# Kernel optimization log

Hardware: AMD Instinct MI355X
Metric: run time of the kernel (lower is better)

The kernel has to match this reference:

```python
import jax, jax.numpy as jnp
import numpy as np

GN_EPS = 1e-5
GN_GROUPS = 8
KNN_EPS = 1e-8


def group_norm(x, w, b):
    # x: [B, C, N]
    B, C, N = x.shape
    xg = x.reshape(B, GN_GROUPS, C // GN_GROUPS, N)
    mu = jnp.mean(xg, axis=(2, 3), keepdims=True)
    var = jnp.var(xg, axis=(2, 3), keepdims=True)
    xg = (xg - mu) * jax.lax.rsqrt(var + GN_EPS)
    return xg.reshape(B, C, N) * w[None, :, None] + b[None, :, None]


def swish(x):
    return x * jax.nn.sigmoid(x)


def three_interpolate(points_coords, centers_coords, centers_features):
    # points_coords [B,3,N], centers_coords [B,3,M], centers_features [B,C,M]
    B, _, N = points_coords.shape
    C = centers_features.shape[1]
    p2 = jnp.sum(points_coords ** 2, axis=1)            # [B,N]
    c2 = jnp.sum(centers_coords ** 2, axis=1)           # [B,M]
    cross = jnp.einsum('bdn,bdm->bnm', points_coords, centers_coords)
    dist2 = p2[:, :, None] + c2[:, None, :] - 2.0 * cross  # [B,N,M] squared dists
    neg_d, idx = jax.lax.top_k(-dist2, 3)               # 3 smallest -> [B,N,3]
    d = -neg_d
    w = 1.0 / (d + KNN_EPS)
    w = w / jnp.sum(w, axis=-1, keepdims=True)          # [B,N,3]
    featsT = jnp.swapaxes(centers_features, 1, 2)       # [B,M,C]
    gathered = jnp.take_along_axis(featsT, idx.reshape(B, N * 3, 1), axis=1)
    gathered = gathered.reshape(B, N, 3, C)
    out = jnp.einsum('bnk,bnkc->bcn', w, gathered)      # [B,C,N]
    return out


def setup_inputs() -> dict:
    key = jax.random.key(0)
    ks = jax.random.split(key, 8)
    B, N, M = 8, 8192, 2048
    C_ctr, C_pts, D = 256, 128, 64
    Cin, C1, C2 = C_ctr + C_pts, 256, 256
    return {
        'points_coords': jax.random.normal(ks[0], (B, 3, N), jnp.float32),
        'centers_coords': jax.random.normal(ks[1], (B, 3, M), jnp.float32),
        'centers_features': jax.random.normal(ks[2], (B, C_ctr, M), jnp.float32),
        'points_features': jax.random.normal(ks[3], (B, C_pts, N), jnp.float32),
        'time_emb': jax.random.normal(ks[4], (B, D, 1), jnp.float32),
        'W1': jax.random.normal(ks[5], (C1, Cin), jnp.float32) * (1.0 / np.sqrt(Cin)),
        'b1': jnp.zeros((C1,), jnp.float32),
        'gn1_w': jnp.ones((C1,), jnp.float32),
        'gn1_b': jnp.zeros((C1,), jnp.float32),
        'W2': jax.random.normal(ks[6], (C2, C1), jnp.float32) * (1.0 / np.sqrt(C1)),
        'b2': jnp.zeros((C2,), jnp.float32),
        'gn2_w': jnp.ones((C2,), jnp.float32),
        'gn2_b': jnp.zeros((C2,), jnp.float32),
    }


def reference(points_coords, centers_coords, centers_features, points_features,
              time_emb, W1, b1, gn1_w, gn1_b, W2, b2, gn2_w, gn2_b):
    interp = three_interpolate(points_coords, centers_coords, centers_features)
    x = jnp.concatenate([interp, points_features], axis=1)  # [B, Cin, N]
    # SharedMLP layer 1: Conv1d(k=1) + GroupNorm(8) + Swish
    x = jnp.einsum('oc,bcn->bon', W1, x) + b1[None, :, None]
    x = swish(group_norm(x, gn1_w, gn1_b))
    # layer 2
    x = jnp.einsum('oc,bcn->bon', W2, x) + b2[None, :, None]
    x = swish(group_norm(x, gn2_w, gn2_b))
    N = points_coords.shape[-1]
    time_emb_exp = jnp.broadcast_to(time_emb[:, :, 0:1], time_emb.shape[:2] + (N,))
    return (x, points_coords, time_emb_exp)
```

## Files before the change

kernel.cpp:

```cpp
#include <hip/hip_runtime.h>
#include <hip/hip_bf16.h>
#include <float.h>

#define B_ 8
#define N_ 8192
#define M_ 2048
#define CC_ 256
#define CP_ 128
#define CIN_ 384
#define GRP_ 8

typedef __attribute__((ext_vector_type(8))) short short8;
typedef __attribute__((ext_vector_type(4))) short short4v;
typedef __attribute__((ext_vector_type(4))) float f32x4;

static __device__ __forceinline__ float bf2f(unsigned short u) {
  union { unsigned int i; float f; } v; v.i = ((unsigned int)u) << 16; return v.f;
}
static __device__ __forceinline__ unsigned short f2bf(float f) {
  union { float f; unsigned int i; } v; v.f = f;
  unsigned int u = v.i;
  unsigned int r = (u + 0x7FFFu + ((u >> 16) & 1u)) >> 16;
  return (unsigned short)r;
}
static __device__ __forceinline__ void gload16(const void* g, void* l) {
  __builtin_amdgcn_global_load_lds(
      (const __attribute__((address_space(1))) void*)g,
      (__attribute__((address_space(3))) void*)l, 16, 0, 0);
}

__global__ __launch_bounds__(256) void k_prep(
    const float* __restrict__ W1, const float* __restrict__ W2,
    short* __restrict__ W1b, short* __restrict__ W2b,
    const float* __restrict__ cf, short* __restrict__ FT,
    const float* __restrict__ pf, short* __restrict__ x0T) {
  __shared__ float tile[32][33];
  int bid = blockIdx.x;
  int t = threadIdx.x;
  if (bid < 384) {
    int i = bid * 256 + t;
    if (i < 256 * CIN_) W1b[i] = (short)f2bf(W1[i]);
    if (i < 256 * 256)  W2b[i] = (short)f2bf(W2[i]);
    return;
  }
  const float* in; short* out;
  int C, Nn, RS, coff, n0, c0, b;
  if (bid < 4480) {
    int q = bid - 384;
    in = cf; out = FT; C = CC_; Nn = M_; RS = CC_; coff = 0;
    n0 = (q & 63) * 32; c0 = ((q >> 6) & 7) * 32; b = q >> 9;
  } else {
    int q = bid - 4480;
    in = pf; out = x0T; C = CP_; Nn = N_; RS = CIN_; coff = 256;
    n0 = (q & 255) * 32; c0 = ((q >> 8) & 3) * 32; b = q >> 10;
  }
  const float* inb = in + (size_t)b * C * Nn;
  short* outb = out + (size_t)b * Nn * RS;
  int tx = t & 31, ty = t >> 5;
#pragma unroll
  for (int i = 0; i < 32; i += 8)
    tile[ty + i][tx] = inb[(size_t)(c0 + ty + i) * Nn + n0 + tx];
  __syncthreads();
#pragma unroll
  for (int i = 0; i < 32; i += 8)
    outb[(size_t)(n0 + ty + i) * RS + coff + c0 + tx] = (short)f2bf(tile[tx][ty + i]);
}

__global__ __launch_bounds__(512) void k_knn(
    const float* __restrict__ pc, const float* __restrict__ cc,
    int* __restrict__ idx, float* __restrict__ wts) {
  __shared__ __align__(16) float4 ctr[M_];
  __shared__ double mk[8][3][128];
  int b = blockIdx.y;
  int t = threadIdx.x;
  const float* ccb = cc + (size_t)b * 3 * M_;
  for (int i = t; i < M_; i += 512) {
    float x = ccb[i], y = ccb[M_ + i], z = ccb[2 * M_ + i];
    ctr[i] = make_float4(x, y, z, x * x + y * y + z * z);
  }
  __syncthreads();
  int wv = t >> 6, lane = t & 63;
  int base = blockIdx.x * 128;
  const float* pcb = pc + (size_t)b * 3 * N_;
  int na = base + lane, nb = base + 64 + lane;
  float pxa = pcb[na], pya = pcb[N_ + na], pza = pcb[2 * N_ + na];
  float pxb = pcb[nb], pyb = pcb[N_ + nb], pzb = pcb[2 * N_ + nb];
  float p2a = pxa * pxa + pya * pya + pza * pza;
  float p2b = pxb * pxb + pyb * pyb + pzb * pzb;
  const double kinit = __hiloint2double(0x7F7FFFFF, 0);
  double a0 = kinit, a1 = kinit, a2 = kinit;
  double e0 = kinit, e1 = kinit, e2 = kinit;
  const float4* C = ctr + wv * 256;
  int mbase = wv * 256;
#pragma unroll 8
  for (int m = 0; m < 256; ++m) {
    float4 c = C[m];
    float dota = pxa * c.x;
    dota = __builtin_fmaf(pya, c.y, dota);
    dota = __builtin_fmaf(pza, c.z, dota);
    float da = __builtin_fmaf(-2.f, dota, c.w) + p2a;
    float dotb = pxb * c.x;
    dotb = __builtin_fmaf(pyb, c.y, dotb);
    dotb = __builtin_fmaf(pzb, c.z, dotb);
    float db = __builtin_fmaf(-2.f, dotb, c.w) + p2b;
    double ka = __hiloint2double(__float_as_int(da), mbase + m);
    double kb = __hiloint2double(__float_as_int(db), mbase + m);
    double t0 = fmin(ka, a0);
    double t1 = fmin(fmax(ka, a0), a1);
    double t2 = fmin(fmax(ka, a1), a2);
    a0 = t0; a1 = t1; a2 = t2;
    double u0 = fmin(kb, e0);
    double u1 = fmin(fmax(kb, e0), e1);
    double u2 = fmin(fmax(kb, e1), e2);
    e0 = u0; e1 = u1; e2 = u2;
  }
  mk[wv][0][lane] = a0; mk[wv][1][lane] = a1; mk[wv][2][lane] = a2;
  mk[wv][0][64 + lane] = e0; mk[wv][1][64 + lane] = e1; mk[wv][2][64 + lane] = e2;
  __syncthreads();
  if (t < 128) {
    double k0 = kinit, k1 = kinit, k2 = kinit;
#pragma unroll
    for (int w = 0; w < 8; ++w) {
#pragma unroll
      for (int j = 0; j < 3; ++j) {
        double key = mk[w][j][t];
        double n0 = fmin(key, k0);
        double n1 = fmin(fmax(key, k0), k1);
        double n2 = fmin(fmax(key, k1), k2);
        k0 = n0; k1 = n1; k2 = n2;
      }
    }
    float d0 = __int_as_float(__double2hiint(k0));
    float d1 = __int_as_float(__double2hiint(k1));
    float d2 = __int_as_float(__double2hiint(k2));
    float w0 = 1.f / (d0 + 1e-8f), w1 = 1.f / (d1 + 1e-8f), w2 = 1.f / (d2 + 1e-8f);
    float inv = 1.f / (w0 + w1 + w2);
    int bn = b * N_ + base + t;
    wts[bn] = w0 * inv; wts[B_ * N_ + bn] = w1 * inv; wts[2 * B_ * N_ + bn] = w2 * inv;
    idx[bn] = __double2loint(k0);
    idx[B_ * N_ + bn] = __double2loint(k1);
    idx[2 * B_ * N_ + bn] = __double2loint(k2);
  }
}

__global__ __launch_bounds__(256) void k_interp(
    const short* __restrict__ FT, const int* __restrict__ idx,
    const float* __restrict__ wts, short* __restrict__ x0T) {
  int b = blockIdx.y;
  int t = threadIdx.x;
  int nl = t >> 5, cch = (t & 31) * 8;
  int n = blockIdx.x * 8 + nl;
  int bn = b * N_ + n;
  int i0 = idx[bn], i1 = idx[B_ * N_ + bn], i2 = idx[2 * B_ * N_ + bn];
  float w0 = wts[bn], w1 = wts[B_ * N_ + bn], w2 = wts[2 * B_ * N_ + bn];
  const short* Fb = FT + (size_t)b * M_ * CC_;
  short8 f0 = *(const short8*)(Fb + (size_t)i0 * CC_ + cch);
  short8 f1 = *(const short8*)(Fb + (size_t)i1 * CC_ + cch);
  short8 f2 = *(const short8*)(Fb + (size_t)i2 * CC_ + cch);
  short8 r;
#pragma unroll
  for (int e = 0; e < 8; ++e) {
    float v = w0 * bf2f((unsigned short)f0[e]) + w1 * bf2f((unsigned short)f1[e]) +
              w2 * bf2f((unsigned short)f2[e]);
    r[e] = (short)f2bf(v);
  }
  *(short8*)(x0T + (size_t)bn * CIN_ + cch) = r;
}

__global__ __launch_bounds__(256) void k_gemm(
    const short* __restrict__ Wb, const short* __restrict__ Xb,
    const float* __restrict__ bias, short* __restrict__ Yb,
    float* __restrict__ part, int K) {
  __shared__ __align__(16) short sW[128 * 64];
  __shared__ __align__(16) short sX[128 * 64];
  int b = blockIdx.z;
  int otile = blockIdx.x * 128;
  int ntile = blockIdx.y * 128;
  int t = threadIdx.x;
  int wv = t >> 6, lane = t & 63;
  int wr = wv >> 1, wc = wv & 1;
  int fr = lane & 15;
  int g = lane >> 4;
  f32x4 acc[4][4] = {};
  const short* Wp = Wb + (size_t)otile * K;
  const short* Xp = Xb + ((size_t)b * N_ + ntile) * K;
  for (int k0 = 0; k0 < K; k0 += 64) {
#pragma unroll
    for (int j = 0; j < 4; ++j) {
      int s = j * 256 + t;
      int row = s >> 3;
      int kc = (s & 7) ^ (row & 7);
      gload16(Wp + (size_t)row * K + k0 + kc * 8, sW + j * 2048 + wv * 512);
      gload16(Xp + (size_t)row * K + k0 + kc * 8, sX + j * 2048 + wv * 512);
    }
    __syncthreads();
#pragma unroll
    for (int h = 0; h < 2; ++h) {
      short8 af[4], bfr[4];
#pragma unroll
      for (int m = 0; m < 4; ++m) {
        int ra = wr * 64 + m * 16 + fr;
        af[m] = *(const short8*)(sW + ra * 64 + (((h * 4 + g) ^ (ra & 7)) << 3));
        int rb = wc * 64 + m * 16 + fr;
        bfr[m] = *(const short8*)(sX + rb * 64 + (((h * 4 + g) ^ (rb & 7)) << 3));
      }
#pragma unroll
      for (int m = 0; m < 4; ++m)
#pragma unroll
        for (int nn = 0; nn < 4; ++nn)
          acc[m][nn] = __builtin_amdgcn_mfma_f32_16x16x32_bf16(af[m], bfr[nn], acc[m][nn], 0, 0, 0);
    }
    __syncthreads();
  }
  float s01 = 0.f, ss01 = 0.f, s23 = 0.f, ss23 = 0.f;
#pragma unroll
  for (int m = 0; m < 4; ++m) {
    int o = otile + wr * 64 + m * 16 + g * 4;
    float4 bi = *(const float4*)(bias + o);
#pragma unroll
    for (int nn = 0; nn < 4; ++nn) {
      int n = ntile + wc * 64 + nn * 16 + fr;
      float v0 = acc[m][nn][0] + bi.x;
      float v1 = acc[m][nn][1] + bi.y;
      float v2 = acc[m][nn][2] + bi.z;
      float v3 = acc[m][nn][3] + bi.w;
      if (m < 2) { s01 += v0 + v1 + v2 + v3; ss01 += v0*v0 + v1*v1 + v2*v2 + v3*v3; }
      else       { s23 += v0 + v1 + v2 + v3; ss23 += v0*v0 + v1*v1 + v2*v2 + v3*v3; }
      short4v sv;
      sv[0] = (short)f2bf(v0);
      sv[1] = (short)f2bf(v1);
      sv[2] = (short)f2bf(v2);
      sv[3] = (short)f2bf(v3);
      *(short4v*)(Yb + ((size_t)b * N_ + n) * 256 + o) = sv;
    }
  }
#pragma unroll
  for (int off = 32; off > 0; off >>= 1) {
    s01 += __shfl_down(s01, off);
    ss01 += __shfl_down(ss01, off);
    s23 += __shfl_down(s23, off);
    ss23 += __shfl_down(ss23, off);
  }
  float* wred = (float*)sW;
  if (lane == 0) {
    wred[wv * 4 + 0] = s01; wred[wv * 4 + 1] = ss01;
    wred[wv * 4 + 2] = s23; wred[wv * 4 + 3] = ss23;
  }
  __syncthreads();
  if (t < 8) {
    int gl = t >> 1, sel = t & 1;
    int wrn = gl >> 1;
    int id = (gl & 1) * 2 + sel;
    float v = wred[(wrn * 2 + 0) * 4 + id] + wred[(wrn * 2 + 1) * 4 + id];
    part[(((size_t)b * 8 + blockIdx.x * 4 + gl) * 64 + blockIdx.y) * 2 + sel] = v;
  }
}

__global__ __launch_bounds__(256) void k_gnapply(short* __restrict__ Y,
                                                 const float* __restrict__ part,
                                                 const float* __restrict__ gw,
                                                 const float* __restrict__ gb) {
  __shared__ float fs[128];
  int t = threadIdx.x;
  if (t < 64) {
    float s = 0.f, ss = 0.f;
    for (int j = 0; j < 64; ++j) {
      s += part[((size_t)t * 64 + j) * 2];
      ss += part[((size_t)t * 64 + j) * 2 + 1];
    }
    const float cnt = 32.f * 8192.f;
    float mean = s / cnt;
    float var = ss / cnt - mean * mean;
    fs[t * 2] = mean;
    fs[t * 2 + 1] = rsqrtf(var + 1e-5f);
  }
  __syncthreads();
  unsigned int* Yd = (unsigned int*)Y;
  int total = B_ * N_ * 128;
  for (int i = blockIdx.x * blockDim.x + t; i < total;
       i += gridDim.x * blockDim.x) {
    int o2 = i & 127;
    int b = i >> 20;
    int g = o2 >> 4;
    float mean = fs[(b * 8 + g) * 2], rstd = fs[(b * 8 + g) * 2 + 1];
    unsigned int v = Yd[i];
    int o = o2 * 2;
    float a = bf2f((unsigned short)(v & 0xFFFF));
    float c = bf2f((unsigned short)(v >> 16));
    a = (a - mean) * rstd * gw[o] + gb[o];
    c = (c - mean) * rstd * gw[o + 1] + gb[o + 1];
    a = a / (1.f + __expf(-a));
    c = c / (1.f + __expf(-c));
    Yd[i] = (unsigned int)f2bf(a) | ((unsigned int)f2bf(c) << 16);
  }
}

__global__ __launch_bounds__(256) void k_gnapply_out(
    const short* __restrict__ Y, const float* __restrict__ part,
    const float* __restrict__ gw, const float* __restrict__ gb,
    float* __restrict__ out) {
  __shared__ float tile[64][65];
  __shared__ float fs[16];
  int b = blockIdx.z;
  int t = threadIdx.x;
  if (t < 8) {
    float s = 0.f, ss = 0.f;
    for (int j = 0; j < 64; ++j) {
      s += part[(((size_t)b * 8 + t) * 64 + j) * 2];
      ss += part[(((size_t)b * 8 + t) * 64 + j) * 2 + 1];
    }
    const float cnt = 32.f * 8192.f;
    float mean = s / cnt;
    float var = ss / cnt - mean * mean;
    fs[t * 2] = mean;
    fs[t * 2 + 1] = rsqrtf(var + 1e-5f);
  }
  __syncthreads();
  int n0 = blockIdx.x * 64, o0 = blockIdx.y * 64;
  int row = t >> 5, dcol = t & 31;
  const unsigned int* Yd = (const unsigned int*)(Y + (size_t)b * N_ * 256);
  int o = o0 + dcol * 2;
  int g = o >> 5;
  float mean = fs[g * 2], rstd = fs[g * 2 + 1];
  float w0 = gw[o], w1 = gw[o + 1], bb0 = gb[o], bb1 = gb[o + 1];
#pragma unroll
  for (int p = 0; p < 8; ++p) {
    int n = n0 + p * 8 + row;
    unsigned int v = Yd[(size_t)n * 128 + (o0 >> 1) + dcol];
    float a = bf2f((unsigned short)(v & 0xFFFF));
    float c = bf2f((unsigned short)(v >> 16));
    a = (a - mean) * rstd * w0 + bb0; a = a / (1.f + __expf(-a));
    c = (c - mean) * rstd * w1 + bb1; c = c / (1.f + __expf(-c));
    tile[p * 8 + row][dcol * 2] = a;
    tile[p * 8 + row][dcol * 2 + 1] = c;
  }
  __syncthreads();
  int ol = t >> 2, nch = (t & 3) * 16;
  float* ob = out + ((size_t)(b * 256 + o0 + ol)) * N_ + n0 + nch;
#pragma unroll
  for (int c4 = 0; c4 < 16; c4 += 4) {
    float4 v4;
    v4.x = tile[nch + c4 + 0][ol];
    v4.y = tile[nch + c4 + 1][ol];
    v4.z = tile[nch + c4 + 2][ol];
    v4.w = tile[nch + c4 + 3][ol];
    *(float4*)(ob + c4) = v4;
  }
}

__global__ void k_tail(const float* __restrict__ pc, const float* __restrict__ te,
                       float* __restrict__ out) {
  int total = 196608 + B_ * 64 * N_;
  for (int i = blockIdx.x * blockDim.x + threadIdx.x; i < total;
       i += gridDim.x * blockDim.x) {
    if (i < 196608) {
      out[16777216 + i] = pc[i];
    } else {
      int j = i - 196608;
      int bd = j >> 13;
      out[16973824 + j] = te[bd];
    }
  }
}

extern "C" void kernel_launch(void* const* d_in, const int* in_sizes, int n_in,
                              void* d_out, int out_size, void* d_ws, size_t ws_size,
                              hipStream_t stream) {
  const float* pc  = (const float*)d_in[0];
  const float* cc  = (const float*)d_in[1];
  const float* cf  = (const float*)d_in[2];
  const float* pf  = (const float*)d_in[3];
  const float* te  = (const float*)d_in[4];
  const float* W1  = (const float*)d_in[5];
  const float* b1  = (const float*)d_in[6];
  const float* g1w = (const float*)d_in[7];
  const float* g1b = (const float*)d_in[8];
  const float* W2  = (const float*)d_in[9];
  const float* b2  = (const float*)d_in[10];
  const float* g2w = (const float*)d_in[11];
  const float* g2b = (const float*)d_in[12];
  float* out = (float*)d_out;

  char* ws = (char*)d_ws;
  size_t off = 0;
  auto alloc = [&](size_t bytes) {
    char* p = ws + off;
    off += (bytes + 255) & ~(size_t)255;
    return p;
  };
  short* FT   = (short*)alloc((size_t)B_ * M_ * CC_ * 2);
  short* x0T  = (short*)alloc((size_t)B_ * N_ * CIN_ * 2);
  short* y1   = (short*)alloc((size_t)B_ * N_ * 256 * 2);
  short* W1b  = (short*)alloc(256 * 384 * 2);
  short* W2b  = (short*)alloc(256 * 256 * 2);
  int*   idx  = (int*)alloc((size_t)3 * B_ * N_ * 4);
  float* wts  = (float*)alloc((size_t)3 * B_ * N_ * 4);
  float* part1 = (float*)alloc(8 * 8 * 64 * 2 * 4);
  float* part2 = (float*)alloc(8 * 8 * 64 * 2 * 4);
  short* y2 = (short*)x0T;

  k_prep<<<12672, 256, 0, stream>>>(W1, W2, W1b, W2b, cf, FT, pf, x0T);
  k_knn<<<dim3(N_ / 128, B_), 512, 0, stream>>>(pc, cc, idx, wts);
  k_interp<<<dim3(N_ / 8, B_), 256, 0, stream>>>(FT, idx, wts, x0T);
  k_gemm<<<dim3(2, N_ / 128, B_), 256, 0, stream>>>(W1b, x0T, b1, y1, part1, CIN_);
  k_gnapply<<<2048, 256, 0, stream>>>(y1, part1, g1w, g1b);
  k_gemm<<<dim3(2, N_ / 128, B_), 256, 0, stream>>>(W2b, y1, b2, y2, part2, 256);
  k_gnapply_out<<<dim3(N_ / 64, 4, B_), 256, 0, stream>>>(y2, part2, g2w, g2b, out);
  k_tail<<<2048, 256, 0, stream>>>(pc, te, out);
}
```

Measured before the change: 194.8 us.

## Merge prep, kNN and tail copy into one heterogeneous front kernel

Combines the weight/feature conversion, the kNN search and the passthrough output copy into a single launch, with the work type chosen by block index. Independent work can then share the GPU at once, which removes two launch gaps and lets the memory-bound transposes run beside the compute-bound kNN. In exchange every block reserves the union shared-memory footprint (56KB) and uses 512 threads, which can lower occupancy for the transpose blocks. The transpose now packs two 32x32 tiles per block.

```diff
diff --git a/kernel.cpp b/kernel.cpp
--- a/kernel.cpp
+++ b/kernel.cpp
@@ -29,117 +29,128 @@
       (__attribute__((address_space(3))) void*)l, 16, 0, 0);
 }
 
-__global__ __launch_bounds__(256) void k_prep(
+__global__ __launch_bounds__(512) void k_front(
+    const float* __restrict__ pc, const float* __restrict__ cc,
+    int* __restrict__ idx, float* __restrict__ wts,
     const float* __restrict__ W1, const float* __restrict__ W2,
     short* __restrict__ W1b, short* __restrict__ W2b,
     const float* __restrict__ cf, short* __restrict__ FT,
-    const float* __restrict__ pf, short* __restrict__ x0T) {
-  __shared__ float tile[32][33];
+    const float* __restrict__ pf, short* __restrict__ x0T,
+    const float* __restrict__ te, float* __restrict__ out) {
+  __shared__ __align__(16) char smem[57344];
   int bid = blockIdx.x;
   int t = threadIdx.x;
-  if (bid < 384) {
-    int i = bid * 256 + t;
+  if (bid < 512) {
+    float4* ctr = (float4*)smem;
+    double (*mk)[3][128] = (double(*)[3][128])(smem + 32768);
+    int b = bid >> 6;
+    int base = (bid & 63) * 128;
+    const float* ccb = cc + (size_t)b * 3 * M_;
+    for (int i = t; i < M_; i += 512) {
+      float x = ccb[i], y = ccb[M_ + i], z = ccb[2 * M_ + i];
+      ctr[i] = make_float4(x, y, z, x * x + y * y + z * z);
+    }
+    __syncthreads();
+    int wv = t >> 6, lane = t & 63;
+    const float* pcb = pc + (size_t)b * 3 * N_;
+    int na = base + lane, nb = base + 64 + lane;
+    float pxa = pcb[na], pya = pcb[N_ + na], pza = pcb[2 * N_ + na];
+    float pxb = pcb[nb], pyb = pcb[N_ + nb], pzb = pcb[2 * N_ + nb];
+    float p2a = pxa * pxa + pya * pya + pza * pza;
+    float p2b = pxb * pxb + pyb * pyb + pzb * pzb;
+    const double kinit = __hiloint2double(0x7F7FFFFF, 0);
+    double a0 = kinit, a1 = kinit, a2 = kinit;
+    double e0 = kinit, e1 = kinit, e2 = kinit;
+    const float4* C = ctr + wv * 256;
+    int mbase = wv * 256;
+#pragma unroll 8
+    for (int m = 0; m < 256; ++m) {
+      float4 c = C[m];
+      float dota = pxa * c.x;
+      dota = __builtin_fmaf(pya, c.y, dota);
+      dota = __builtin_fmaf(pza, c.z, dota);
+      float da = __builtin_fmaf(-2.f, dota, c.w) + p2a;
+      float dotb = pxb * c.x;
+      dotb = __builtin_fmaf(pyb, c.y, dotb);
+      dotb = __builtin_fmaf(pzb, c.z, dotb);
+      float db = __builtin_fmaf(-2.f, dotb, c.w) + p2b;
+      double ka = __hiloint2double(__float_as_int(da), mbase + m);
+      double kb = __hiloint2double(__float_as_int(db), mbase + m);
+      double t0 = fmin(ka, a0);
+      double t1 = fmin(fmax(ka, a0), a1);
+      double t2 = fmin(fmax(ka, a1), a2);
+      a0 = t0; a1 = t1; a2 = t2;
+      double u0 = fmin(kb, e0);
+      double u1 = fmin(fmax(kb, e0), e1);
+      double u2 = fmin(fmax(kb, e1), e2);
+      e0 = u0; e1 = u1; e2 = u2;
+    }
+    mk[wv][0][lane] = a0; mk[wv][1][lane] = a1; mk[wv][2][lane] = a2;
+    mk[wv][0][64 + lane] = e0; mk[wv][1][64 + lane] = e1; mk[wv][2][64 + lane] = e2;
+    __syncthreads();
+    if (t < 128) {
+      double k0 = kinit, k1 = kinit, k2 = kinit;
+#pragma unroll
+      for (int w = 0; w < 8; ++w) {
+#pragma unroll
+        for (int j = 0; j < 3; ++j) {
+          double key = mk[w][j][t];
+          double n0 = fmin(key, k0);
+          double n1 = fmin(fmax(key, k0), k1);
+          double n2 = fmin(fmax(key, k1), k2);
+          k0 = n0; k1 = n1; k2 = n2;
+        }
+      }
+      float d0 = __int_as_float(__double2hiint(k0));
+      float d1 = __int_as_float(__double2hiint(k1));
+      float d2 = __int_as_float(__double2hiint(k2));
+      float w0 = 1.f / (d0 + 1e-8f), w1 = 1.f / (d1 + 1e-8f), w2 = 1.f / (d2 + 1e-8f);
+      float inv = 1.f / (w0 + w1 + w2);
+      int bn = b * N_ + base + t;
+      wts[bn] = w0 * inv; wts[B_ * N_ + bn] = w1 * inv; wts[2 * B_ * N_ + bn] = w2 * inv;
+      idx[bn] = __double2loint(k0);
+      idx[B_ * N_ + bn] = __double2loint(k1);
+      idx[2 * B_ * N_ + bn] = __double2loint(k2);
+    }
+  } else if (bid < 704) {
+    int i = (bid - 512) * 512 + t;
     if (i < 256 * CIN_) W1b[i] = (short)f2bf(W1[i]);
     if (i < 256 * 256)  W2b[i] = (short)f2bf(W2[i]);
-    return;
-  }
-  const float* in; short* out;
-  int C, Nn, RS, coff, n0, c0, b;
-  if (bid < 4480) {
-    int q = bid - 384;
-    in = cf; out = FT; C = CC_; Nn = M_; RS = CC_; coff = 0;
-    n0 = (q & 63) * 32; c0 = ((q >> 6) & 7) * 32; b = q >> 9;
+  } else if (bid < 6848) {
+    int q2 = (bid - 704) * 2 + (t >> 8);
+    int tt = t & 255;
+    float (*tile)[33] = (float(*)[33])(smem + (t >> 8) * 4352);
+    const float* in; short* outp;
+    int C, Nn, RS, coff, n0, c0, b;
+    if (q2 < 4096) {
+      in = cf; outp = FT; C = CC_; Nn = M_; RS = CC_; coff = 0;
+      n0 = (q2 & 63) * 32; c0 = ((q2 >> 6) & 7) * 32; b = q2 >> 9;
+    } else {
+      int q = q2 - 4096;
+      in = pf; outp = x0T; C = CP_; Nn = N_; RS = CIN_; coff = 256;
+      n0 = (q & 255) * 32; c0 = ((q >> 8) & 3) * 32; b = q >> 10;
+    }
+    const float* inb = in + (size_t)b * C * Nn;
+    short* outb = outp + (size_t)b * Nn * RS;
+    int tx = tt & 31, ty = tt >> 5;
+#pragma unroll
+    for (int i = 0; i < 32; i += 8)
+      tile[ty + i][tx] = inb[(size_t)(c0 + ty + i) * Nn + n0 + tx];
+    __syncthreads();
+#pragma unroll
+    for (int i = 0; i < 32; i += 8)
+      outb[(size_t)(n0 + ty + i) * RS + coff + c0 + tx] = (short)f2bf(tile[tx][ty + i]);
   } else {
-    int q = bid - 4480;
-    in = pf; out = x0T; C = CP_; Nn = N_; RS = CIN_; coff = 256;
-    n0 = (q & 255) * 32; c0 = ((q >> 8) & 3) * 32; b = q >> 10;
-  }
-  const float* inb = in + (size_t)b * C * Nn;
-  short* outb = out + (size_t)b * Nn * RS;
-  int tx = t & 31, ty = t >> 5;
-#pragma unroll
-  for (int i = 0; i < 32; i += 8)
-    tile[ty + i][tx] = inb[(size_t)(c0 + ty + i) * Nn + n0 + tx];
-  __syncthreads();
-#pragma unroll
-  for (int i = 0; i < 32; i += 8)
-    outb[(size_t)(n0 + ty + i) * RS + coff + c0 + tx] = (short)f2bf(tile[tx][ty + i]);
-}
-
-__global__ __launch_bounds__(512) void k_knn(
-    const float* __restrict__ pc, const float* __restrict__ cc,
-    int* __restrict__ idx, float* __restrict__ wts) {
-  __shared__ __align__(16) float4 ctr[M_];
-  __shared__ double mk[8][3][128];
-  int b = blockIdx.y;
-  int t = threadIdx.x;
-  const float* ccb = cc + (size_t)b * 3 * M_;
-  for (int i = t; i < M_; i += 512) {
-    float x = ccb[i], y = ccb[M_ + i], z = ccb[2 * M_ + i];
-    ctr[i] = make_float4(x, y, z, x * x + y * y + z * z);
-  }
-  __syncthreads();
-  int wv = t >> 6, lane = t & 63;
-  int base = blockIdx.x * 128;
-  const float* pcb = pc + (size_t)b * 3 * N_;
-  int na = base + lane, nb = base + 64 + lane;
-  float pxa = pcb[na], pya = pcb[N_ + na], pza = pcb[2 * N_ + na];
-  float pxb = pcb[nb], pyb = pcb[N_ + nb], pzb = pcb[2 * N_ + nb];
-  float p2a = pxa * pxa + pya * pya + pza * pza;
-  float p2b = pxb * pxb + pyb * pyb + pzb * pzb;
-  const double kinit = __hiloint2double(0x7F7FFFFF, 0);
-  double a0 = kinit, a1 = kinit, a2 = kinit;
-  double e0 = kinit, e1 = kinit, e2 = kinit;
-  const float4* C = ctr + wv * 256;
-  int mbase = wv * 256;
-#pragma unroll 8
-  for (int m = 0; m < 256; ++m) {
-    float4 c = C[m];
-    float dota = pxa * c.x;
-    dota = __builtin_fmaf(pya, c.y, dota);
-    dota = __builtin_fmaf(pza, c.z, dota);
-    float da = __builtin_fmaf(-2.f, dota, c.w) + p2a;
-    float dotb = pxb * c.x;
-    dotb = __builtin_fmaf(pyb, c.y, dotb);
-    dotb = __builtin_fmaf(pzb, c.z, dotb);
-    float db = __builtin_fmaf(-2.f, dotb, c.w) + p2b;
-    double ka = __hiloint2double(__float_as_int(da), mbase + m);
-    double kb = __hiloint2double(__float_as_int(db), mbase + m);
-    double t0 = fmin(ka, a0);
-    double t1 = fmin(fmax(ka, a0), a1);
-    double t2 = fmin(fmax(ka, a1), a2);
-    a0 = t0; a1 = t1; a2 = t2;
-    double u0 = fmin(kb, e0);
-    double u1 = fmin(fmax(kb, e0), e1);
-    double u2 = fmin(fmax(kb, e1), e2);
-    e0 = u0; e1 = u1; e2 = u2;
-  }
-  mk[wv][0][lane] = a0; mk[wv][1][lane] = a1; mk[wv][2][lane] = a2;
-  mk[wv][0][64 + lane] = e0; mk[wv][1][64 + lane] = e1; mk[wv][2][64 + lane] = e2;
-  __syncthreads();
-  if (t < 128) {
-    double k0 = kinit, k1 = kinit, k2 = kinit;
-#pragma unroll
-    for (int w = 0; w < 8; ++w) {
-#pragma unroll
-      for (int j = 0; j < 3; ++j) {
-        double key = mk[w][j][t];
-        double n0 = fmin(key, k0);
-        double n1 = fmin(fmax(key, k0), k1);
-        double n2 = fmin(fmax(key, k1), k2);
-        k0 = n0; k1 = n1; k2 = n2;
+    int total = 196608 + B_ * 64 * N_;
+    for (int i = (bid - 6848) * 512 + t; i < total; i += 512 * 512) {
+      if (i < 196608) {
+        out[16777216 + i] = pc[i];
+      } else {
+        int j = i - 196608;
+        int bd = j >> 13;
+        out[16973824 + j] = te[bd];
       }
     }
-    float d0 = __int_as_float(__double2hiint(k0));
-    float d1 = __int_as_float(__double2hiint(k1));
-    float d2 = __int_as_float(__double2hiint(k2));
-    float w0 = 1.f / (d0 + 1e-8f), w1 = 1.f / (d1 + 1e-8f), w2 = 1.f / (d2 + 1e-8f);
-    float inv = 1.f / (w0 + w1 + w2);
-    int bn = b * N_ + base + t;
-    wts[bn] = w0 * inv; wts[B_ * N_ + bn] = w1 * inv; wts[2 * B_ * N_ + bn] = w2 * inv;
-    idx[bn] = __double2loint(k0);
-    idx[B_ * N_ + bn] = __double2loint(k1);
-    idx[2 * B_ * N_ + bn] = __double2loint(k2);
   }
 }
 
@@ -348,21 +359,6 @@
   }
 }
 
-__global__ void k_tail(const float* __restrict__ pc, const float* __restrict__ te,
-                       float* __restrict__ out) {
-  int total = 196608 + B_ * 64 * N_;
-  for (int i = blockIdx.x * blockDim.x + threadIdx.x; i < total;
-       i += gridDim.x * blockDim.x) {
-    if (i < 196608) {
-      out[16777216 + i] = pc[i];
-    } else {
-      int j = i - 196608;
-      int bd = j >> 13;
-      out[16973824 + j] = te[bd];
-    }
-  }
-}
-
 extern "C" void kernel_launch(void* const* d_in, const int* in_sizes, int n_in,
                               void* d_out, int out_size, void* d_ws, size_t ws_size,
                               hipStream_t stream) {
@@ -399,12 +395,11 @@
   float* part2 = (float*)alloc(8 * 8 * 64 * 2 * 4);
   short* y2 = (short*)x0T;
 
-  k_prep<<<12672, 256, 0, stream>>>(W1, W2, W1b, W2b, cf, FT, pf, x0T);
-  k_knn<<<dim3(N_ / 128, B_), 512, 0, stream>>>(pc, cc, idx, wts);
+  k_front<<<7360, 512, 0, stream>>>(pc, cc, idx, wts, W1, W2, W1b, W2b,
+                                    cf, FT, pf, x0T, te, out);
   k_interp<<<dim3(N_ / 8, B_), 256, 0, stream>>>(FT, idx, wts, x0T);
   k_gemm<<<dim3(2, N_ / 128, B_), 256, 0, stream>>>(W1b, x0T, b1, y1, part1, CIN_);
   k_gnapply<<<2048, 256, 0, stream>>>(y1, part1, g1w, g1b);
   k_gemm<<<dim3(2, N_ / 128, B_), 256, 0, stream>>>(W2b, y1, b2, y2, part2, 256);
   k_gnapply_out<<<dim3(N_ / 64, 4, B_), 256, 0, stream>>>(y2, part2, g2w, g2b, out);
-  k_tail<<<2048, 256, 0, stream>>>(pc, te, out);
-}
+}
```

Result: no change. 191.2 us (-1.9%).
